# Kernel tuning notes

Measured on AMD Instinct MI355X. Metric: run time of the kernel, lower is better.

## Reference

```python
import jax, jax.numpy as jnp
import numpy as np

B = 2
ROW, COL = 63, 84          # resolution
ROW_, COL_ = 32, 42        # resolution_
N = ROW * COL              # 5292 kv tokens
N_ = ROW_ * COL_           # 1344 q tokens
IN_DIM, OUT_DIM = 256, 512
KEY_DIM, NUM_HEADS, ATTN_RATIO, STRIDE = 16, 8, 2, 2
D = ATTN_RATIO * KEY_DIM   # 32 (value dim per head)
DH = D * NUM_HEADS         # 256
NH_KD = KEY_DIM * NUM_HEADS  # 128
H_KV = DH + NH_KD          # 384
SCALE = KEY_DIM ** -0.5
EPS = 1e-5


def _build_bias_idxs():
    # replicates the itertools.product double loop, vectorized; ids ordered by
    # first occurrence in row-major scan (same as dict insertion order).
    r_ = np.arange(ROW_); c_ = np.arange(COL_)
    r = np.arange(ROW); c = np.arange(COL)
    off_r = np.abs(r_[:, None] * STRIDE - r[None, :])      # (32, 63)
    off_c = np.abs(c_[:, None] * STRIDE - c[None, :])      # (42, 84)
    keys = (off_r[:, None, :, None] * 1000 + off_c[None, :, None, :]).reshape(-1)
    _, first_idx, inv = np.unique(keys, return_index=True, return_inverse=True)
    order = np.argsort(first_idx)
    rank = np.empty_like(order); rank[order] = np.arange(len(order))
    idxs = rank[inv].reshape(N_, N).astype(np.int32)
    return idxs, len(order)


def setup_inputs() -> dict:
    key = jax.random.key(0)
    ks = jax.random.split(key, 12)
    idxs_np, n_off = _build_bias_idxs()
    inp = {
        "x": jax.random.normal(ks[0], (B, N, IN_DIM), jnp.float32),
        "kv_w": jax.random.normal(ks[1], (H_KV, IN_DIM), jnp.float32) * (IN_DIM ** -0.5),
        "kv_g": jnp.ones((H_KV,), jnp.float32),
        "kv_b": jnp.zeros((H_KV,), jnp.float32),
        "q_w": jax.random.normal(ks[2], (NH_KD, IN_DIM), jnp.float32) * (IN_DIM ** -0.5),
        "q_g": jnp.ones((NH_KD,), jnp.float32),
        "q_b": jnp.zeros((NH_KD,), jnp.float32),
        "proj_w": jax.random.normal(ks[3], (OUT_DIM, DH), jnp.float32) * (DH ** -0.5),
        "proj_g": jnp.ones((OUT_DIM,), jnp.float32),
        "proj_b": jnp.zeros((OUT_DIM,), jnp.float32),
        "bias_table": jax.random.normal(ks[4], (NUM_HEADS, n_off), jnp.float32) * 0.02,
        "bias_idxs": jnp.asarray(idxs_np),
    }
    return inp


def _linear_bn(x, w, g, b):
    # Linear (no bias) followed by BatchNorm1d in training mode (batch stats
    # over flattened (B*N) dim, biased variance).
    y = jnp.einsum("bnc,oc->bno", x, w)
    flat = y.reshape(-1, y.shape[-1])
    mu = flat.mean(0)
    var = flat.var(0)
    return (y - mu) * (g / jnp.sqrt(var + EPS)) + b


def _hardswish(x):
    return x * jnp.clip(x + 3.0, 0.0, 6.0) / 6.0


def reference(x, kv_w, kv_g, kv_b, q_w, q_g, q_b, proj_w, proj_g, proj_b,
              bias_table, bias_idxs):
    Bx = x.shape[0]
    # kv projection -> split k (KEY_DIM) and v (D) per head
    kv = _linear_bn(x, kv_w, kv_g, kv_b).reshape(Bx, N, NUM_HEADS, KEY_DIM + D)
    k = kv[..., :KEY_DIM].transpose(0, 2, 1, 3)   # (B, H, N, key_dim)
    v = kv[..., KEY_DIM:].transpose(0, 2, 1, 3)   # (B, H, N, d)
    # q: spatial subsample then projection
    xs = x.reshape(Bx, ROW, COL, IN_DIM)[:, ::STRIDE, ::STRIDE].reshape(Bx, N_, IN_DIM)
    q = _linear_bn(xs, q_w, q_g, q_b).reshape(Bx, N_, NUM_HEADS, KEY_DIM).transpose(0, 2, 1, 3)
    # gathered relative position bias: (H, N_, N)
    ab = bias_table[:, bias_idxs]
    attn = jnp.einsum("bhqd,bhkd->bhqk", q, k) * SCALE + ab[None]
    attn = jax.nn.softmax(attn, axis=-1)
    out = jnp.einsum("bhqk,bhkd->bhqd", attn, v)       # (B, H, N_, d)
    out = out.transpose(0, 2, 1, 3).reshape(Bx, N_, DH)
    out = _linear_bn(_hardswish(out), proj_w, proj_g, proj_b)
    return out
```

## Files before the change

kernel.cpp:

```cpp
#include <hip/hip_runtime.h>
#include <hip/hip_bf16.h>
#include <math.h>

#define N_K 5292
#define N_KP 5376
#define N_Q 1344
#define NH_KD 128
#define NROWS 21504
#define LOG2E 1.4426950408889634f
#define MSTAT 16.0f

typedef float f32x4 __attribute__((ext_vector_type(4)));
typedef short short8 __attribute__((ext_vector_type(8)));

__device__ __forceinline__ float fexp2(float x) {
#if __has_builtin(__builtin_amdgcn_exp2f)
    return __builtin_amdgcn_exp2f(x);
#else
    return exp2f(x);
#endif
}

__device__ __forceinline__ unsigned pk_bf16(float a, float b) {
    union { __hip_bfloat162 h; unsigned u; } c;
    c.h = __float22bfloat162_rn(make_float2(a, b));
    return c.u;
}
__device__ __forceinline__ unsigned short f2bf(float a) {
    return (unsigned short)pk_bf16(a, 0.f);
}

__global__ __launch_bounds__(256) void prep_kernel(
    const float* __restrict__ bias_table, const int* __restrict__ bias_idxs, int n_off,
    float* __restrict__ zbase, unsigned* __restrict__ Vpt32, float* __restrict__ bt_r)
{
    int bid = blockIdx.x;
    const int t = threadIdx.x;
    if (bid < 8) {
        int i = bid * 256 + t;
        if (i < 2048) zbase[i] = 0.f;
        return;
    }
    bid -= 8;
    if (bid < 128) {
        int i = bid * 256 + t;
        int row = i >> 6, c = i & 63;
        Vpt32[(size_t)row * (N_KP / 2) + (5248 / 2) + c] = 0u;
        return;
    }
    bid -= 128;
    {
        int i = bid * 256 + t;
        if (i < 8 * N_K) {
            int h = i / N_K, j = i - h * N_K;
            bt_r[i] = bias_table[h * n_off + bias_idxs[j]] * LOG2E;
        }
    }
}

__device__ __forceinline__ void gemm_body_f32(
    const float* __restrict__ A, const float* __restrict__ W,
    long asrc, int nrow,
    unsigned short (*As)[40], unsigned short (*Bs)[40], f32x4 acc[4])
{
    const int t = threadIdx.x;
    const int w = t >> 6, lane = t & 63, g = lane >> 4, ln = lane & 15;
    const int srow = t >> 2;
    const int sc8 = (t & 3) * 8;

    for (int k0 = 0; k0 < 256; k0 += 32) {
        uint4 a = make_uint4(0, 0, 0, 0);
        if (asrc >= 0) {
            float4 a0 = *(const float4*)(A + asrc * 256 + k0 + sc8);
            float4 a1 = *(const float4*)(A + asrc * 256 + k0 + sc8 + 4);
            a = make_uint4(pk_bf16(a0.x, a0.y), pk_bf16(a0.z, a0.w),
                           pk_bf16(a1.x, a1.y), pk_bf16(a1.z, a1.w));
        }
        float4 b0 = *(const float4*)(W + (size_t)nrow * 256 + k0 + sc8);
        float4 b1 = *(const float4*)(W + (size_t)nrow * 256 + k0 + sc8 + 4);
        uint4 b = make_uint4(pk_bf16(b0.x, b0.y), pk_bf16(b0.z, b0.w),
                             pk_bf16(b1.x, b1.y), pk_bf16(b1.z, b1.w));

        __syncthreads();
        *(uint4*)&As[srow][sc8] = a;
        *(uint4*)&Bs[srow][sc8] = b;
        __syncthreads();

        short8 ah = *(const short8*)&As[w * 16 + ln][g * 8];
        #pragma unroll
        for (int nt = 0; nt < 4; ++nt) {
            short8 bh = *(const short8*)&Bs[nt * 16 + ln][g * 8];
            acc[nt] = __builtin_amdgcn_mfma_f32_16x16x32_bf16(ah, bh, acc[nt], 0, 0, 0);
        }
    }
}

__device__ __forceinline__ void gemm_body_bf16(
    const unsigned short* __restrict__ A, const float* __restrict__ W,
    long asrc, int nrow,
    unsigned short (*As)[40], unsigned short (*Bs)[40], f32x4 acc[4])
{
    const int t = threadIdx.x;
    const int w = t >> 6, lane = t & 63, g = lane >> 4, ln = lane & 15;
    const int srow = t >> 2;
    const int sc8 = (t & 3) * 8;

    for (int k0 = 0; k0 < 256; k0 += 32) {
        uint4 a = *(const uint4*)(A + asrc * 256 + k0 + sc8);
        float4 b0 = *(const float4*)(W + (size_t)nrow * 256 + k0 + sc8);
        float4 b1 = *(const float4*)(W + (size_t)nrow * 256 + k0 + sc8 + 4);
        uint4 b = make_uint4(pk_bf16(b0.x, b0.y), pk_bf16(b0.z, b0.w),
                             pk_bf16(b1.x, b1.y), pk_bf16(b1.z, b1.w));

        __syncthreads();
        *(uint4*)&As[srow][sc8] = a;
        *(uint4*)&Bs[srow][sc8] = b;
        __syncthreads();

        short8 ah = *(const short8*)&As[w * 16 + ln][g * 8];
        #pragma unroll
        for (int nt = 0; nt < 4; ++nt) {
            short8 bh = *(const short8*)&Bs[nt * 16 + ln][g * 8];
            acc[nt] = __builtin_amdgcn_mfma_f32_16x16x32_bf16(ah, bh, acc[nt], 0, 0, 0);
        }
    }
}

__device__ __forceinline__ void gemm_stats(f32x4 acc[4], float* __restrict__ sums,
                                           int n0, int Ncols, float* scratch)
{
    const int t = threadIdx.x;
    const int w = t >> 6, lane = t & 63, g = lane >> 4, ln = lane & 15;
    float s4[4], q4[4];
    #pragma unroll
    for (int nt = 0; nt < 4; ++nt) {
        float s = acc[nt][0] + acc[nt][1] + acc[nt][2] + acc[nt][3];
        float q = fmaf(acc[nt][0], acc[nt][0], fmaf(acc[nt][1], acc[nt][1],
                  fmaf(acc[nt][2], acc[nt][2], acc[nt][3] * acc[nt][3])));
        s += __shfl_xor(s, 16); s += __shfl_xor(s, 32);
        q += __shfl_xor(q, 16); q += __shfl_xor(q, 32);
        s4[nt] = s; q4[nt] = q;
    }
    __syncthreads();
    float* st_s = scratch;
    float* st_q = scratch + 256;
    if (g == 0) {
        #pragma unroll
        for (int nt = 0; nt < 4; ++nt) {
            st_s[(w * 4 + nt) * 16 + ln] = s4[nt];
            st_q[(w * 4 + nt) * 16 + ln] = q4[nt];
        }
    }
    __syncthreads();
    if (t < 64) {
        int nt = t >> 4, c = t & 15;
        float a = 0.f, b2 = 0.f;
        #pragma unroll
        for (int ww = 0; ww < 4; ++ww) {
            a  += st_s[(ww * 4 + nt) * 16 + c];
            b2 += st_q[(ww * 4 + nt) * 16 + c];
        }
        atomicAdd(&sums[n0 + nt * 16 + c], a);
        atomicAdd(&sums[Ncols + n0 + nt * 16 + c], b2);
    }
}

__global__ __launch_bounds__(256) void gemm_qkv(
    const float* __restrict__ X, const float* __restrict__ kv_w, const float* __restrict__ q_w,
    unsigned short* __restrict__ Kp, unsigned short* __restrict__ Vpt,
    float* __restrict__ q_y, float* __restrict__ sums_kv, float* __restrict__ sums_q)
{
    __shared__ unsigned short As[64][40], Bs[64][40];
    const int t = threadIdx.x;
    const int w = t >> 6, lane = t & 63, g = lane >> 4, ln = lane & 15;
    const int srow = t >> 2;
    int id = blockIdx.x;

    f32x4 acc[4];
    #pragma unroll
    for (int nt = 0; nt < 4; ++nt) acc[nt] = (f32x4){0.f, 0.f, 0.f, 0.f};

    if (id < 1008) {
        const int xcd = id & 7, id8 = id >> 3;
        const int my = xcd + (id8 / 6) * 8, ny = id8 % 6;
        if (my >= 166) return;
        const int m0 = my * 64, n0 = ny * 64;
        int mrow = m0 + srow;
        long asrc = (mrow < 10584) ? mrow : -1;
        gemm_body_f32(X, kv_w, asrc, n0 + srow, As, Bs, acc);

        #pragma unroll
        for (int nt = 0; nt < 4; ++nt) {
            int c = n0 + nt * 16 + ln;
            int hh = c / 48, cc = c - 48 * hh;
            #pragma unroll
            for (int reg = 0; reg < 4; ++reg) {
                int mr = m0 + w * 16 + g * 4 + reg;
                if (mr < 10584) {
                    int bb = mr >= N_K;
                    int key = mr - bb * N_K;
                    unsigned short v16 = f2bf(acc[nt][reg]);
                    if (cc < 16) {
                        Kp[((size_t)(bb * 8 + hh) * N_K + key) * 16 + cc] = v16;
                    } else {
                        int kap = key & 63;
                        int keyp = (key & ~63) | (((kap & 15) << 2) | (kap >> 4));
                        Vpt[((size_t)(bb * 8 + hh) * 32 + cc - 16) * N_KP + keyp] = v16;
                    }
                }
            }
        }
        gemm_stats(acc, sums_kv, n0, 384, (float*)&As[0][0]);
    } else {
        id -= 1008;
        const int xcd = id & 7, id8 = id >> 3;
        const int my = xcd + (id8 / 2) * 8, ny = id8 % 2;
        if (my >= 42) return;
        const int m0 = my * 64, n0 = ny * 64;
        int mrow = m0 + srow;
        int bb = mrow / N_Q;
        int i = mrow - bb * N_Q;
        long asrc = (long)(bb * N_K + (i / 42) * 168 + (i % 42) * 2);
        gemm_body_f32(X, q_w, asrc, n0 + srow, As, Bs, acc);

        #pragma unroll
        for (int nt = 0; nt < 4; ++nt)
            #pragma unroll
            for (int reg = 0; reg < 4; ++reg) {
                int mr = m0 + w * 16 + g * 4 + reg;
                q_y[(size_t)mr * 128 + n0 + nt * 16 + ln] = acc[nt][reg];
            }
        gemm_stats(acc, sums_q, n0, 128, (float*)&As[0][0]);
    }
}

__global__ __launch_bounds__(256) void gemm_proj(
    const unsigned short* __restrict__ Ap, const float* __restrict__ Wp,
    float* __restrict__ Y, float* __restrict__ sums)
{
    __shared__ unsigned short As[64][40], Bs[64][40];
    const int t = threadIdx.x;
    const int w = t >> 6, lane = t & 63, g = lane >> 4, ln = lane & 15;
    const int id = blockIdx.x;
    const int xcd = id & 7, id8 = id >> 3;
    const int my = xcd + (id8 / 8) * 8, ny = id8 % 8;
    if (my >= 42) return;
    const int m0 = my * 64, n0 = ny * 64;

    f32x4 acc[4];
    #pragma unroll
    for (int nt = 0; nt < 4; ++nt) acc[nt] = (f32x4){0.f, 0.f, 0.f, 0.f};
    gemm_body_bf16(Ap, Wp, m0 + (t >> 2), n0 + (t >> 2), As, Bs, acc);

    #pragma unroll
    for (int nt = 0; nt < 4; ++nt)
        #pragma unroll
        for (int reg = 0; reg < 4; ++reg) {
            int mr = m0 + w * 16 + g * 4 + reg;
            Y[(size_t)mr * 512 + n0 + nt * 16 + ln] = acc[nt][reg];
        }
    gemm_stats(acc, sums, n0, 512, (float*)&As[0][0]);
}

__global__ __launch_bounds__(256, 5) void attn_mfma(
    const unsigned short* __restrict__ Kp, const unsigned short* __restrict__ Vpt,
    const float* __restrict__ q_y, const float* __restrict__ sums_q,
    const float* __restrict__ q_g, const float* __restrict__ q_b,
    const float* __restrict__ sums_kv, const float* __restrict__ kv_g,
    const float* __restrict__ bt_r,
    float* __restrict__ pl, float* __restrict__ pacc)
{
    const int id = blockIdx.x;
    const int h = id & 7;
    const int z = (id >> 3) & 7;
    const int qt = id >> 6;
    const int b = z >> 2, ks = z & 3;
    const int t = threadIdx.x;
    const int w = t >> 6, lane = t & 63, g = lane >> 4, ln = lane & 15;

    __shared__ unsigned short btm_s[21 * 166];
    __shared__ unsigned short K_s[2][64][24];
    __shared__ unsigned short Vt_s[2][32][72];
    __shared__ unsigned short P_s[4][16][72];

    const int q0 = qt * 64;
    const int kstart = ks * 1344;
    const int kend = (kstart + 1344 < N_K) ? kstart + 1344 : N_K;
    const int ntiles = (kend - kstart + 63) >> 6;
    const bool tail = (ks == 3);

    const int kr0 = kstart / 84;
    const int kr1 = (kend - 1) / 84;
    const int rq2min = (q0 / 42) * 2;
    const int rq2max = ((q0 + 63) / 42) * 2;
    const int dmin_r = rq2min - kr1;
    const int rows = (rq2max - kr0) - dmin_r + 1;
    const int nb = rows * 166;
    const int mx = nb - 1;
    {
        const float* src = bt_r + h * N_K;
        for (int j = t; j < nb; j += 256) {
            int rr = j / 166, ii = j - rr * 166;
            int dr = dmin_r + rr; dr = dr < 0 ? -dr : dr;
            int dc = ii - 83; dc = dc < 0 ? -dc : dc;
            btm_s[j] = f2bf(src[dr * 84 + dc]);
        }
    }

    short8 qfrag = (short8)0;
    if (lane < 32) {
        const float invq = 1.f / 2688.f, invk = 1.f / 10584.f;
        const float post = 0.25f * LOG2E;
        const int c0 = h * 16 + g * 8;
        const int ck = h * 48 + g * 8;
        const float* qp = q_y + (size_t)(b * N_Q + q0 + w * 16 + ln) * NH_KD + c0;
        float vv[8];
        #pragma unroll
        for (int j = 0; j < 8; ++j) {
            float mu  = sums_q[c0 + j] * invq;
            float var = fmaf(-mu, mu, sums_q[128 + c0 + j] * invq);
            float s   = q_g[c0 + j] * rsqrtf(var + 1e-5f) * post;
            float vq  = fmaf(qp[j], s, fmaf(-mu, s, q_b[c0 + j] * post));
            float muk = sums_kv[ck + j] * invk;
            float vrk = fmaf(-muk, muk, sums_kv[384 + ck + j] * invk);
            float sk  = kv_g[ck + j] * rsqrtf(vrk + 1e-5f);
            vv[j] = vq * sk;
        }
        union { short8 s; unsigned u[4]; } qf;
        qf.u[0] = pk_bf16(vv[0], vv[1]); qf.u[1] = pk_bf16(vv[2], vv[3]);
        qf.u[2] = pk_bf16(vv[4], vv[5]); qf.u[3] = pk_bf16(vv[6], vv[7]);
        qfrag = qf.s;
    }

    int base[4];
    #pragma unroll
    for (int reg = 0; reg < 4; ++reg) {
        int qg = q0 + w * 16 + g * 4 + reg;
        int rq2 = (qg / 42) * 2;
        int cq2 = (qg % 42) * 2;
        base[reg] = (rq2 - dmin_r) * 166 + cq2 + 83;
    }
    int off[4], kcc[4];
    #pragma unroll
    for (int st = 0; st < 4; ++st) {
        int kg = kstart + st * 16 + ln;
        int okr = kg / 84;
        kcc[st] = kg - okr * 84;
        off[st] = -(okr * 166 + kcc[st]);
    }

    const unsigned* kp_base = (const unsigned*)Kp + (size_t)(b * 8 + h) * N_K * 8;
    const unsigned short* vp_base = Vpt + (size_t)(b * 8 + h) * 32 * N_KP;
    const int skey = t >> 2, schunk = t & 3;
    const int vrow = t >> 3, vc8 = (t & 7) * 8;

    uint2 kreg; uint4 vreg;
    {
        int kg = kstart + skey; if (kg > N_K - 1) kg = N_K - 1;
        kreg = *(const uint2*)(kp_base + (size_t)kg * 8 + schunk * 2);
        vreg = *(const uint4*)(vp_base + (size_t)vrow * N_KP + kstart + vc8);
    }
    *(uint2*)&K_s[0][skey][schunk * 4] = kreg;
    *(uint4*)&Vt_s[0][vrow][vc8] = vreg;
    __syncthreads();

    float l[4] = {0.f, 0.f, 0.f, 0.f};
    f32x4 acc0 = {0.f, 0.f, 0.f, 0.f}, acc1 = {0.f, 0.f, 0.f, 0.f};
    const f32x4 minit = {-MSTAT, -MSTAT, -MSTAT, -MSTAT};
    int p = 0;

    for (int it = 0; it < ntiles; ++it) {
        const int k0 = kstart + it * 64;
        const bool notlast = (it + 1 < ntiles);
        if (notlast) {
            int kg = k0 + 64 + skey; if (kg > N_K - 1) kg = N_K - 1;
            kreg = *(const uint2*)(kp_base + (size_t)kg * 8 + schunk * 2);
            vreg = *(const uint4*)(vp_base + (size_t)vrow * N_KP + k0 + 64 + vc8);
        }

        f32x4 sf[4];
        #pragma unroll
        for (int st = 0; st < 4; ++st) {
            short8 bf = (short8)0;
            if (lane < 32) bf = *(const short8*)&K_s[p][st * 16 + ln][g * 8];
            sf[st] = __builtin_amdgcn_mfma_f32_16x16x32_bf16(qfrag, bf, minit, 0, 0, 0);
        }

        float pv[4][4];
        #pragma unroll
        for (int st = 0; st < 4; ++st) {
            #pragma unroll
            for (int reg = 0; reg < 4; ++reg) {
                int idx = base[reg] + off[st];
                idx = idx < 0 ? 0 : idx;
                idx = idx > mx ? mx : idx;
                float bias = __uint_as_float(((unsigned)btm_s[idx]) << 16);
                pv[st][reg] = fexp2(sf[st][reg] + bias);
            }
        }
        if (tail && it == ntiles - 1) {
            #pragma unroll
            for (int st = 0; st < 4; ++st) {
                bool bad = (k0 + st * 16 + ln) >= N_K;
                #pragma unroll
                for (int reg = 0; reg < 4; ++reg)
                    pv[st][reg] = bad ? 0.f : pv[st][reg];
            }
        }

        #pragma unroll
        for (int reg = 0; reg < 4; ++reg) {
            l[reg] += (pv[0][reg] + pv[1][reg]) + (pv[2][reg] + pv[3][reg]);
            uint2 pw = make_uint2(pk_bf16(pv[0][reg], pv[1][reg]),
                                  pk_bf16(pv[2][reg], pv[3][reg]));
            *(uint2*)&P_s[w][g * 4 + reg][4 * ln] = pw;
        }
        __asm__ __volatile__("" ::: "memory");

        #pragma unroll
        for (int kt = 0; kt < 2; ++kt) {
            short8 af = *(const short8*)&P_s[w][ln][g * 8 + kt * 32];
            short8 b0 = *(const short8*)&Vt_s[p][ln][g * 8 + kt * 32];
            short8 b1 = *(const short8*)&Vt_s[p][ln + 16][g * 8 + kt * 32];
            acc0 = __builtin_amdgcn_mfma_f32_16x16x32_bf16(af, b0, acc0, 0, 0, 0);
            acc1 = __builtin_amdgcn_mfma_f32_16x16x32_bf16(af, b1, acc1, 0, 0, 0);
        }

        if (notlast) {
            int q2 = p ^ 1;
            *(uint2*)&K_s[q2][skey][schunk * 4] = kreg;
            *(uint4*)&Vt_s[q2][vrow][vc8] = vreg;
            __syncthreads();
            p = q2;
        }

        #pragma unroll
        for (int st = 0; st < 4; ++st) {
            kcc[st] += 64;
            if (kcc[st] >= 84) { kcc[st] -= 84; off[st] -= 146; }
            else off[st] -= 64;
        }
    }

    #pragma unroll
    for (int reg = 0; reg < 4; ++reg) {
        float s = l[reg];
        s += __shfl_xor(s, 1, 16);
        s += __shfl_xor(s, 2, 16);
        s += __shfl_xor(s, 4, 16);
        s += __shfl_xor(s, 8, 16);
        l[reg] = s;
    }

    const int rbase = (b * 8 + h) * N_Q + q0 + w * 16;
    #pragma unroll
    for (int reg = 0; reg < 4; ++reg) {
        int prow = ks * NROWS + rbase + g * 4 + reg;
        pacc[(size_t)prow * 32 + ln]      = acc0[reg];
        pacc[(size_t)prow * 32 + 16 + ln] = acc1[reg];
        if (ln == 0) pl[prow] = l[reg];
    }
}

__global__ __launch_bounds__(256) void combine_kernel(const float* __restrict__ pl,
                                                      const float* __restrict__ pacc,
                                                      const float* __restrict__ sums_kv,
                                                      const float* __restrict__ kv_g,
                                                      const float* __restrict__ kv_b,
                                                      unsigned short* __restrict__ attn_o)
{
    int idx = blockIdx.x * 256 + threadIdx.x;
    int r = idx >> 3, e4 = (idx & 7) * 4;
    float L = (pl[r] + pl[NROWS + r]) + (pl[2 * NROWS + r] + pl[3 * NROWS + r]);
    float invL = 1.f / L;
    size_t o = (size_t)r * 32 + e4;
    float4 v0 = *(const float4*)(pacc + o);
    float4 v1 = *(const float4*)(pacc + (size_t)NROWS * 32 + o);
    float4 v2 = *(const float4*)(pacc + (size_t)2 * NROWS * 32 + o);
    float4 v3 = *(const float4*)(pacc + (size_t)3 * NROWS * 32 + o);
    int q = r % N_Q;
    int bh = r / N_Q;
    int hh = bh & 7, b = bh >> 3;
    const int ch = hh * 48 + 16 + e4;
    const float invk = 1.f / 10584.f;
    float hs[4];
    #pragma unroll
    for (int u = 0; u < 4; ++u) {
        float v = (u == 0 ? v0.x + v1.x + v2.x + v3.x :
                   u == 1 ? v0.y + v1.y + v2.y + v3.y :
                   u == 2 ? v0.z + v1.z + v2.z + v3.z :
                            v0.w + v1.w + v2.w + v3.w);
        float mu  = sums_kv[ch + u] * invk;
        float var = fmaf(-mu, mu, sums_kv[384 + ch + u] * invk);
        float s   = kv_g[ch + u] * rsqrtf(var + 1e-5f);
        float tt  = fmaf(-mu, s, kv_b[ch + u]);
        v = fmaf(s, v * invL, tt);
        hs[u] = v * fminf(fmaxf(v + 3.f, 0.f), 6.f) * (1.f / 6.f);
    }
    *(uint2*)(attn_o + (size_t)(b * N_Q + q) * 256 + hh * 32 + e4) =
        make_uint2(pk_bf16(hs[0], hs[1]), pk_bf16(hs[2], hs[3]));
}

__global__ __launch_bounds__(256) void norm_apply(
    const float* __restrict__ Y, const float* __restrict__ sums,
    const float* __restrict__ g, const float* __restrict__ bb,
    float* __restrict__ out, int rows, int cols, float inv_rows)
{
    __shared__ float sc_s[64], sh_s[64];
    const int t = threadIdx.x;
    const int c0 = blockIdx.x * 64;
    if (t < 64) {
        int c = c0 + t;
        float mu  = sums[c] * inv_rows;
        float var = fmaf(-mu, mu, sums[cols + c] * inv_rows);
        float s   = g[c] * rsqrtf(var + 1e-5f);
        sc_s[t] = s;
        sh_s[t] = fmaf(-mu, s, bb[c]);
    }
    __syncthreads();
    const int c4 = (t & 15) * 4;
    float4 scv = *(const float4*)&sc_s[c4];
    float4 shv = *(const float4*)&sh_s[c4];
    for (int r = blockIdx.y * 16 + (t >> 4); r < rows; r += gridDim.y * 16) {
        size_t off = (size_t)r * cols + c0 + c4;
        float4 v = *(const float4*)(Y + off);
        v.x = fmaf(v.x, scv.x, shv.x);
        v.y = fmaf(v.y, scv.y, shv.y);
        v.z = fmaf(v.z, scv.z, shv.z);
        v.w = fmaf(v.w, scv.w, shv.w);
        *(float4*)(out + off) = v;
    }
}

extern "C" void kernel_launch(void* const* d_in, const int* in_sizes, int n_in,
                              void* d_out, int out_size, void* d_ws, size_t ws_size,
                              hipStream_t stream) {
    (void)n_in; (void)out_size; (void)ws_size;
    const float* x      = (const float*)d_in[0];
    const float* kv_w   = (const float*)d_in[1];
    const float* kv_g   = (const float*)d_in[2];
    const float* kv_b   = (const float*)d_in[3];
    const float* q_w    = (const float*)d_in[4];
    const float* q_g    = (const float*)d_in[5];
    const float* q_b    = (const float*)d_in[6];
    const float* proj_w = (const float*)d_in[7];
    const float* proj_g = (const float*)d_in[8];
    const float* proj_b = (const float*)d_in[9];
    const float* bias_table = (const float*)d_in[10];
    const int*   bias_idxs  = (const int*)d_in[11];
    const int    n_off = in_sizes[10] / 8;
    float* out = (float*)d_out;

    float* ws = (float*)d_ws;
    float* q_y  = ws;
    float* pacc = q_y + 2688 * 128;
    float* proj_y = pacc;
    float* pl = pacc + 4 * NROWS * 32;
    unsigned short* attn_o = (unsigned short*)(pl + 4 * NROWS);
    unsigned short* Kp  = attn_o + 2688 * 256;
    unsigned short* Vpt = Kp + 2 * 8 * N_K * 16;
    float* zbase   = (float*)(Vpt + 2 * 8 * 32 * N_KP);
    float* sums_kv = zbase;
    float* sums_q  = sums_kv + 768;
    float* sums_p  = sums_q + 256;
    float* bt_r    = sums_p + 1024;

    prep_kernel<<<302, 256, 0, stream>>>(bias_table, bias_idxs, n_off, zbase,
                                         (unsigned*)Vpt, bt_r);
    gemm_qkv<<<1104, 256, 0, stream>>>(x, kv_w, q_w, Kp, Vpt, q_y, sums_kv, sums_q);
    attn_mfma<<<1344, 256, 0, stream>>>(Kp, Vpt, q_y, sums_q, q_g, q_b,
                                        sums_kv, kv_g, bt_r, pl, pacc);
    combine_kernel<<<672, 256, 0, stream>>>(pl, pacc, sums_kv, kv_g, kv_b, attn_o);
    gemm_proj<<<384, 256, 0, stream>>>(attn_o, proj_w, proj_y, sums_p);
    norm_apply<<<dim3(8, 84), 256, 0, stream>>>(proj_y, sums_p, proj_g, proj_b, out,
                                                2688, 512, 1.f / 2688.f);
}
```

Baseline: 198.8 us.

## Fuse split-K combine into attention; load K/V fragments directly from global

Restructures the attention kernel so each block takes 16 queries, with its four waves splitting the key range. Partial sums are reduced in shared memory and the BN/hardswish epilogue is applied in the same kernel, which removes the separate combine kernel and the global pacc/pl round trip. K/V fragments are loaded straight from global memory into registers with ping-pong double buffering, replacing the LDS staging and its per-tile barriers. The prep kernel is folded into extra blocks of the QKV GEMM that prebuild a bf16 bias matrix in global memory, and the stats buffer is cleared with a memset. The trade-offs are more global K/V traffic per block, a larger bias LDS footprint, and occupancy lowered from 5 to 4.

```diff
diff --git a/kernel.cpp b/kernel.cpp
--- a/kernel.cpp
+++ b/kernel.cpp
@@ -6,9 +6,9 @@
 #define N_KP 5376
 #define N_Q 1344
 #define NH_KD 128
-#define NROWS 21504
 #define LOG2E 1.4426950408889634f
 #define MSTAT 16.0f
+#define BTM_H 20750
 
 typedef float f32x4 __attribute__((ext_vector_type(4)));
 typedef short short8 __attribute__((ext_vector_type(8)));
@@ -28,34 +28,6 @@
 }
 __device__ __forceinline__ unsigned short f2bf(float a) {
     return (unsigned short)pk_bf16(a, 0.f);
-}
-
-__global__ __launch_bounds__(256) void prep_kernel(
-    const float* __restrict__ bias_table, const int* __restrict__ bias_idxs, int n_off,
-    float* __restrict__ zbase, unsigned* __restrict__ Vpt32, float* __restrict__ bt_r)
-{
-    int bid = blockIdx.x;
-    const int t = threadIdx.x;
-    if (bid < 8) {
-        int i = bid * 256 + t;
-        if (i < 2048) zbase[i] = 0.f;
-        return;
-    }
-    bid -= 8;
-    if (bid < 128) {
-        int i = bid * 256 + t;
-        int row = i >> 6, c = i & 63;
-        Vpt32[(size_t)row * (N_KP / 2) + (5248 / 2) + c] = 0u;
-        return;
-    }
-    bid -= 128;
-    {
-        int i = bid * 256 + t;
-        if (i < 8 * N_K) {
-            int h = i / N_K, j = i - h * N_K;
-            bt_r[i] = bias_table[h * n_off + bias_idxs[j]] * LOG2E;
-        }
-    }
 }
 
 __device__ __forceinline__ void gemm_body_f32(
@@ -167,7 +139,9 @@
 
 __global__ __launch_bounds__(256) void gemm_qkv(
     const float* __restrict__ X, const float* __restrict__ kv_w, const float* __restrict__ q_w,
+    const float* __restrict__ bias_table, const int* __restrict__ bias_idxs, int n_off,
     unsigned short* __restrict__ Kp, unsigned short* __restrict__ Vpt,
+    unsigned short* __restrict__ btm_g,
     float* __restrict__ q_y, float* __restrict__ sums_kv, float* __restrict__ sums_q)
 {
     __shared__ unsigned short As[64][40], Bs[64][40];
@@ -175,6 +149,32 @@
     const int w = t >> 6, lane = t & 63, g = lane >> 4, ln = lane & 15;
     const int srow = t >> 2;
     int id = blockIdx.x;
+
+    if (id >= 1104) {
+        id -= 1104;
+        if (id < 168) {
+            int i = id * 256 + t;
+            int row = i / 84, j = i - row * 84;
+            int slot;
+            if (j < 20) {
+                int kap = 44 + j;
+                slot = 5248 + (((kap & 15) << 2) | (kap >> 4));
+            } else {
+                slot = 5312 + (j - 20);
+            }
+            Vpt[(size_t)row * N_KP + slot] = 0;
+        } else {
+            int i = (id - 168) * 256 + t;
+            if (i < 8 * BTM_H) {
+                int h = i / BTM_H, r = i - h * BTM_H;
+                int dri = r / 166, dci = r - dri * 166;
+                int dr = dri - 62; dr = dr < 0 ? -dr : dr;
+                int dc = dci - 83; dc = dc < 0 ? -dc : dc;
+                btm_g[i] = f2bf(bias_table[h * n_off + bias_idxs[dr * 84 + dc]] * LOG2E);
+            }
+        }
+        return;
+    }
 
     f32x4 acc[4];
     #pragma unroll
@@ -262,49 +262,116 @@
     gemm_stats(acc, sums, n0, 512, (float*)&As[0][0]);
 }
 
-__global__ __launch_bounds__(256, 5) void attn_mfma(
+
+struct Frags { short8 kf[4]; short8 v0[2]; short8 v1[2]; };
+
+__device__ __forceinline__ void load_frags(
+    Frags& f, int k0, int lane, int g, int ln,
+    const unsigned short* __restrict__ kp_base,
+    const unsigned short* __restrict__ vrow0,
+    const unsigned short* __restrict__ vrow1)
+{
+    #pragma unroll
+    for (int st = 0; st < 4; ++st) {
+        int kg = k0 + st * 16 + ln;
+        kg = kg > N_K - 1 ? N_K - 1 : kg;
+        f.kf[st] = (lane < 32) ? *(const short8*)(kp_base + (size_t)kg * 16 + g * 8)
+                               : (short8)0;
+    }
+    #pragma unroll
+    for (int kt = 0; kt < 2; ++kt) {
+        f.v0[kt] = *(const short8*)(vrow0 + k0 + kt * 32 + g * 8);
+        f.v1[kt] = *(const short8*)(vrow1 + k0 + kt * 32 + g * 8);
+    }
+}
+
+__device__ __forceinline__ void do_tile(
+    const Frags& f, int k0, bool mask, int kend_mask,
+    const short8& qfrag, const int base[4], int off[4], int kcc[4],
+    const unsigned short* __restrict__ btm_s, int mx,
+    int w, int g, int ln, unsigned short (*P_s)[16][72],
+    float l[4], f32x4& acc0, f32x4& acc1)
+{
+    const f32x4 minit = {-MSTAT, -MSTAT, -MSTAT, -MSTAT};
+    f32x4 sf[4];
+    #pragma unroll
+    for (int st = 0; st < 4; ++st)
+        sf[st] = __builtin_amdgcn_mfma_f32_16x16x32_bf16(qfrag, f.kf[st], minit, 0, 0, 0);
+
+    float pv[4][4];
+    #pragma unroll
+    for (int st = 0; st < 4; ++st) {
+        #pragma unroll
+        for (int reg = 0; reg < 4; ++reg) {
+            int idx = base[reg] + off[st];
+            idx = idx < 0 ? 0 : idx;
+            idx = idx > mx ? mx : idx;
+            float bias = __uint_as_float(((unsigned)btm_s[idx]) << 16);
+            pv[st][reg] = fexp2(sf[st][reg] + bias);
+        }
+    }
+    if (mask) {
+        #pragma unroll
+        for (int st = 0; st < 4; ++st) {
+            bool bad = (k0 + st * 16 + ln) >= kend_mask;
+            #pragma unroll
+            for (int reg = 0; reg < 4; ++reg)
+                pv[st][reg] = bad ? 0.f : pv[st][reg];
+        }
+    }
+
+    #pragma unroll
+    for (int reg = 0; reg < 4; ++reg) {
+        l[reg] += (pv[0][reg] + pv[1][reg]) + (pv[2][reg] + pv[3][reg]);
+        uint2 pw = make_uint2(pk_bf16(pv[0][reg], pv[1][reg]),
+                              pk_bf16(pv[2][reg], pv[3][reg]));
+        *(uint2*)&P_s[w][g * 4 + reg][4 * ln] = pw;
+    }
+    __asm__ __volatile__("" ::: "memory");
+
+    #pragma unroll
+    for (int kt = 0; kt < 2; ++kt) {
+        short8 af = *(const short8*)&P_s[w][ln][g * 8 + kt * 32];
+        acc0 = __builtin_amdgcn_mfma_f32_16x16x32_bf16(af, f.v0[kt], acc0, 0, 0, 0);
+        acc1 = __builtin_amdgcn_mfma_f32_16x16x32_bf16(af, f.v1[kt], acc1, 0, 0, 0);
+    }
+
+    #pragma unroll
+    for (int st = 0; st < 4; ++st) {
+        kcc[st] += 64;
+        if (kcc[st] >= 84) { kcc[st] -= 84; off[st] -= 146; }
+        else off[st] -= 64;
+    }
+}
+
+__global__ __launch_bounds__(256, 4) void attn_mfma(
     const unsigned short* __restrict__ Kp, const unsigned short* __restrict__ Vpt,
     const float* __restrict__ q_y, const float* __restrict__ sums_q,
     const float* __restrict__ q_g, const float* __restrict__ q_b,
     const float* __restrict__ sums_kv, const float* __restrict__ kv_g,
-    const float* __restrict__ bt_r,
-    float* __restrict__ pl, float* __restrict__ pacc)
+    const float* __restrict__ kv_b, const unsigned short* __restrict__ btm_g,
+    unsigned short* __restrict__ attn_o)
 {
     const int id = blockIdx.x;
     const int h = id & 7;
-    const int z = (id >> 3) & 7;
-    const int qt = id >> 6;
-    const int b = z >> 2, ks = z & 3;
+    const int b = (id >> 3) & 1;
+    const int qt = id >> 4;
     const int t = threadIdx.x;
     const int w = t >> 6, lane = t & 63, g = lane >> 4, ln = lane & 15;
 
-    __shared__ unsigned short btm_s[21 * 166];
-    __shared__ unsigned short K_s[2][64][24];
-    __shared__ unsigned short Vt_s[2][32][72];
+    __shared__ unsigned short btm_s[65 * 166];
     __shared__ unsigned short P_s[4][16][72];
 
-    const int q0 = qt * 64;
-    const int kstart = ks * 1344;
-    const int kend = (kstart + 1344 < N_K) ? kstart + 1344 : N_K;
-    const int ntiles = (kend - kstart + 63) >> 6;
-    const bool tail = (ks == 3);
-
-    const int kr0 = kstart / 84;
-    const int kr1 = (kend - 1) / 84;
+    const int q0 = qt * 16;
     const int rq2min = (q0 / 42) * 2;
-    const int rq2max = ((q0 + 63) / 42) * 2;
-    const int dmin_r = rq2min - kr1;
-    const int rows = (rq2max - kr0) - dmin_r + 1;
-    const int nb = rows * 166;
-    const int mx = nb - 1;
+    const int rq2max = ((q0 + 15) / 42) * 2;
+    const int rows = rq2max - rq2min + 63;
+    const int nb2 = rows * 83;
+    const int mx = rows * 166 - 1;
     {
-        const float* src = bt_r + h * N_K;
-        for (int j = t; j < nb; j += 256) {
-            int rr = j / 166, ii = j - rr * 166;
-            int dr = dmin_r + rr; dr = dr < 0 ? -dr : dr;
-            int dc = ii - 83; dc = dc < 0 ? -dc : dc;
-            btm_s[j] = f2bf(src[dr * 84 + dc]);
-        }
+        const unsigned* src = (const unsigned*)(btm_g + h * BTM_H + rq2min * 166);
+        unsigned* dst = (unsigned*)btm_s;
+        for (int j = t; j < nb2; j += 256) dst[j] = src[j];
     }
 
     short8 qfrag = (short8)0;
@@ -313,7 +380,7 @@
         const float post = 0.25f * LOG2E;
         const int c0 = h * 16 + g * 8;
         const int ck = h * 48 + g * 8;
-        const float* qp = q_y + (size_t)(b * N_Q + q0 + w * 16 + ln) * NH_KD + c0;
+        const float* qp = q_y + (size_t)(b * N_Q + q0 + ln) * NH_KD + c0;
         float vv[8];
         #pragma unroll
         for (int j = 0; j < 8; ++j) {
@@ -332,14 +399,20 @@
         qfrag = qf.s;
     }
 
+    const int dmin_r = rq2min - 62;
     int base[4];
     #pragma unroll
     for (int reg = 0; reg < 4; ++reg) {
-        int qg = q0 + w * 16 + g * 4 + reg;
+        int qg = q0 + g * 4 + reg;
         int rq2 = (qg / 42) * 2;
         int cq2 = (qg % 42) * 2;
         base[reg] = (rq2 - dmin_r) * 166 + cq2 + 83;
     }
+
+    const int kstart = w * 1344;
+    const int ntiles = (w < 3) ? 21 : 20;
+    const bool tailw = (w == 3);
+
     int off[4], kcc[4];
     #pragma unroll
     for (int st = 0; st < 4; ++st) {
@@ -349,97 +422,30 @@
         off[st] = -(okr * 166 + kcc[st]);
     }
 
-    const unsigned* kp_base = (const unsigned*)Kp + (size_t)(b * 8 + h) * N_K * 8;
-    const unsigned short* vp_base = Vpt + (size_t)(b * 8 + h) * 32 * N_KP;
-    const int skey = t >> 2, schunk = t & 3;
-    const int vrow = t >> 3, vc8 = (t & 7) * 8;
-
-    uint2 kreg; uint4 vreg;
-    {
-        int kg = kstart + skey; if (kg > N_K - 1) kg = N_K - 1;
-        kreg = *(const uint2*)(kp_base + (size_t)kg * 8 + schunk * 2);
-        vreg = *(const uint4*)(vp_base + (size_t)vrow * N_KP + kstart + vc8);
-    }
-    *(uint2*)&K_s[0][skey][schunk * 4] = kreg;
-    *(uint4*)&Vt_s[0][vrow][vc8] = vreg;
+    const unsigned short* kp_base = Kp + (size_t)(b * 8 + h) * N_K * 16;
+    const unsigned short* vp = Vpt + (size_t)(b * 8 + h) * 32 * N_KP;
+    const unsigned short* vrow0 = vp + (size_t)ln * N_KP;
+    const unsigned short* vrow1 = vp + (size_t)(ln + 16) * N_KP;
+
     __syncthreads();
 
     float l[4] = {0.f, 0.f, 0.f, 0.f};
     f32x4 acc0 = {0.f, 0.f, 0.f, 0.f}, acc1 = {0.f, 0.f, 0.f, 0.f};
-    const f32x4 minit = {-MSTAT, -MSTAT, -MSTAT, -MSTAT};
-    int p = 0;
-
-    for (int it = 0; it < ntiles; ++it) {
-        const int k0 = kstart + it * 64;
-        const bool notlast = (it + 1 < ntiles);
-        if (notlast) {
-            int kg = k0 + 64 + skey; if (kg > N_K - 1) kg = N_K - 1;
-            kreg = *(const uint2*)(kp_base + (size_t)kg * 8 + schunk * 2);
-            vreg = *(const uint4*)(vp_base + (size_t)vrow * N_KP + k0 + 64 + vc8);
-        }
-
-        f32x4 sf[4];
-        #pragma unroll
-        for (int st = 0; st < 4; ++st) {
-            short8 bf = (short8)0;
-            if (lane < 32) bf = *(const short8*)&K_s[p][st * 16 + ln][g * 8];
-            sf[st] = __builtin_amdgcn_mfma_f32_16x16x32_bf16(qfrag, bf, minit, 0, 0, 0);
-        }
-
-        float pv[4][4];
-        #pragma unroll
-        for (int st = 0; st < 4; ++st) {
-            #pragma unroll
-            for (int reg = 0; reg < 4; ++reg) {
-                int idx = base[reg] + off[st];
-                idx = idx < 0 ? 0 : idx;
-                idx = idx > mx ? mx : idx;
-                float bias = __uint_as_float(((unsigned)btm_s[idx]) << 16);
-                pv[st][reg] = fexp2(sf[st][reg] + bias);
-            }
-        }
-        if (tail && it == ntiles - 1) {
-            #pragma unroll
-            for (int st = 0; st < 4; ++st) {
-                bool bad = (k0 + st * 16 + ln) >= N_K;
-                #pragma unroll
-                for (int reg = 0; reg < 4; ++reg)
-                    pv[st][reg] = bad ? 0.f : pv[st][reg];
-            }
-        }
-
-        #pragma unroll
-        for (int reg = 0; reg < 4; ++reg) {
-            l[reg] += (pv[0][reg] + pv[1][reg]) + (pv[2][reg] + pv[3][reg]);
-            uint2 pw = make_uint2(pk_bf16(pv[0][reg], pv[1][reg]),
-                                  pk_bf16(pv[2][reg], pv[3][reg]));
-            *(uint2*)&P_s[w][g * 4 + reg][4 * ln] = pw;
-        }
-        __asm__ __volatile__("" ::: "memory");
-
-        #pragma unroll
-        for (int kt = 0; kt < 2; ++kt) {
-            short8 af = *(const short8*)&P_s[w][ln][g * 8 + kt * 32];
-            short8 b0 = *(const short8*)&Vt_s[p][ln][g * 8 + kt * 32];
-            short8 b1 = *(const short8*)&Vt_s[p][ln + 16][g * 8 + kt * 32];
-            acc0 = __builtin_amdgcn_mfma_f32_16x16x32_bf16(af, b0, acc0, 0, 0, 0);
-            acc1 = __builtin_amdgcn_mfma_f32_16x16x32_bf16(af, b1, acc1, 0, 0, 0);
-        }
-
-        if (notlast) {
-            int q2 = p ^ 1;
-            *(uint2*)&K_s[q2][skey][schunk * 4] = kreg;
-            *(uint4*)&Vt_s[q2][vrow][vc8] = vreg;
-            __syncthreads();
-            p = q2;
-        }
-
-        #pragma unroll
-        for (int st = 0; st < 4; ++st) {
-            kcc[st] += 64;
-            if (kcc[st] >= 84) { kcc[st] -= 84; off[st] -= 146; }
-            else off[st] -= 64;
-        }
+
+    Frags fA, fB;
+    load_frags(fA, kstart, lane, g, ln, kp_base, vrow0, vrow1);
+    int it = 0;
+    while (true) {
+        int k0 = kstart + it * 64;
+        if (it + 1 < ntiles) load_frags(fB, k0 + 64, lane, g, ln, kp_base, vrow0, vrow1);
+        do_tile(fA, k0, tailw && (it == ntiles - 1), N_K, qfrag, base, off, kcc,
+                btm_s, mx, w, g, ln, P_s, l, acc0, acc1);
+        if (++it >= ntiles) break;
+        k0 += 64;
+        if (it + 1 < ntiles) load_frags(fA, k0 + 64, lane, g, ln, kp_base, vrow0, vrow1);
+        do_tile(fB, k0, tailw && (it == ntiles - 1), N_K, qfrag, base, off, kcc,
+                btm_s, mx, w, g, ln, P_s, l, acc0, acc1);
+        if (++it >= ntiles) break;
     }
 
     #pragma unroll
@@ -452,53 +458,45 @@
         l[reg] = s;
     }
 
-    const int rbase = (b * 8 + h) * N_Q + q0 + w * 16;
+    __syncthreads();
+    float* accs = (float*)btm_s;
+    float* ls   = accs + 4 * 16 * 32;
     #pragma unroll
     for (int reg = 0; reg < 4; ++reg) {
-        int prow = ks * NROWS + rbase + g * 4 + reg;
-        pacc[(size_t)prow * 32 + ln]      = acc0[reg];
-        pacc[(size_t)prow * 32 + 16 + ln] = acc1[reg];
-        if (ln == 0) pl[prow] = l[reg];
-    }
-}
-
-__global__ __launch_bounds__(256) void combine_kernel(const float* __restrict__ pl,
-                                                      const float* __restrict__ pacc,
-                                                      const float* __restrict__ sums_kv,
-                                                      const float* __restrict__ kv_g,
-                                                      const float* __restrict__ kv_b,
-                                                      unsigned short* __restrict__ attn_o)
-{
-    int idx = blockIdx.x * 256 + threadIdx.x;
-    int r = idx >> 3, e4 = (idx & 7) * 4;
-    float L = (pl[r] + pl[NROWS + r]) + (pl[2 * NROWS + r] + pl[3 * NROWS + r]);
-    float invL = 1.f / L;
-    size_t o = (size_t)r * 32 + e4;
-    float4 v0 = *(const float4*)(pacc + o);
-    float4 v1 = *(const float4*)(pacc + (size_t)NROWS * 32 + o);
-    float4 v2 = *(const float4*)(pacc + (size_t)2 * NROWS * 32 + o);
-    float4 v3 = *(const float4*)(pacc + (size_t)3 * NROWS * 32 + o);
-    int q = r % N_Q;
-    int bh = r / N_Q;
-    int hh = bh & 7, b = bh >> 3;
-    const int ch = hh * 48 + 16 + e4;
-    const float invk = 1.f / 10584.f;
-    float hs[4];
-    #pragma unroll
-    for (int u = 0; u < 4; ++u) {
-        float v = (u == 0 ? v0.x + v1.x + v2.x + v3.x :
-                   u == 1 ? v0.y + v1.y + v2.y + v3.y :
-                   u == 2 ? v0.z + v1.z + v2.z + v3.z :
-                            v0.w + v1.w + v2.w + v3.w);
-        float mu  = sums_kv[ch + u] * invk;
-        float var = fmaf(-mu, mu, sums_kv[384 + ch + u] * invk);
-        float s   = kv_g[ch + u] * rsqrtf(var + 1e-5f);
-        float tt  = fmaf(-mu, s, kv_b[ch + u]);
-        v = fmaf(s, v * invL, tt);
-        hs[u] = v * fminf(fmaxf(v + 3.f, 0.f), 6.f) * (1.f / 6.f);
-    }
-    *(uint2*)(attn_o + (size_t)(b * N_Q + q) * 256 + hh * 32 + e4) =
-        make_uint2(pk_bf16(hs[0], hs[1]), pk_bf16(hs[2], hs[3]));
+        int qrow = g * 4 + reg;
+        accs[((w * 16 + qrow) * 32) + ln]      = acc0[reg];
+        accs[((w * 16 + qrow) * 32) + 16 + ln] = acc1[reg];
+        if (ln == 0) ls[w * 16 + qrow] = l[reg];
+    }
+    __syncthreads();
+
+    if (t < 128) {
+        int q = t >> 3, e4 = (t & 7) * 4;
+        float L = (ls[q] + ls[16 + q]) + (ls[32 + q] + ls[48 + q]);
+        float invL = 1.f / L;
+        float4 s0 = *(const float4*)&accs[(q)* 32 + e4];
+        float4 s1 = *(const float4*)&accs[(16 + q) * 32 + e4];
+        float4 s2 = *(const float4*)&accs[(32 + q) * 32 + e4];
+        float4 s3 = *(const float4*)&accs[(48 + q) * 32 + e4];
+        const int ch = h * 48 + 16 + e4;
+        const float invk = 1.f / 10584.f;
+        float hs[4];
+        #pragma unroll
+        for (int u = 0; u < 4; ++u) {
+            float v = (u == 0 ? s0.x + s1.x + s2.x + s3.x :
+                       u == 1 ? s0.y + s1.y + s2.y + s3.y :
+                       u == 2 ? s0.z + s1.z + s2.z + s3.z :
+                                s0.w + s1.w + s2.w + s3.w);
+            float mu  = sums_kv[ch + u] * invk;
+            float var = fmaf(-mu, mu, sums_kv[384 + ch + u] * invk);
+            float sc  = kv_g[ch + u] * rsqrtf(var + 1e-5f);
+            float tt  = fmaf(-mu, sc, kv_b[ch + u]);
+            v = fmaf(sc, v * invL, tt);
+            hs[u] = v * fminf(fmaxf(v + 3.f, 0.f), 6.f) * (1.f / 6.f);
+        }
+        *(uint2*)(attn_o + (size_t)(b * N_Q + q0 + q) * 256 + h * 32 + e4) =
+            make_uint2(pk_bf16(hs[0], hs[1]), pk_bf16(hs[2], hs[3]));
+    }
 }
 
 __global__ __launch_bounds__(256) void norm_apply(
@@ -552,25 +550,22 @@
     float* out = (float*)d_out;
 
     float* ws = (float*)d_ws;
-    float* q_y  = ws;
-    float* pacc = q_y + 2688 * 128;
-    float* proj_y = pacc;
-    float* pl = pacc + 4 * NROWS * 32;
-    unsigned short* attn_o = (unsigned short*)(pl + 4 * NROWS);
+    float* q_y    = ws;
+    float* proj_y = q_y + 2688 * 128;
+    unsigned short* attn_o = (unsigned short*)(proj_y + 2688 * 512);
     unsigned short* Kp  = attn_o + 2688 * 256;
     unsigned short* Vpt = Kp + 2 * 8 * N_K * 16;
-    float* zbase   = (float*)(Vpt + 2 * 8 * 32 * N_KP);
-    float* sums_kv = zbase;
+    unsigned short* btm_g = Vpt + 2 * 8 * 32 * N_KP;
+    float* sums_kv = (float*)(btm_g + 8 * BTM_H);
     float* sums_q  = sums_kv + 768;
     float* sums_p  = sums_q + 256;
-    float* bt_r    = sums_p + 1024;
-
-    prep_kernel<<<302, 256, 0, stream>>>(bias_table, bias_idxs, n_off, zbase,
-                                         (unsigned*)Vpt, bt_r);
-    gemm_qkv<<<1104, 256, 0, stream>>>(x, kv_w, q_w, Kp, Vpt, q_y, sums_kv, sums_q);
+
+    hipMemsetAsync(sums_kv, 0, 2048 * sizeof(float), stream);
+    gemm_qkv<<<1104 + 168 + 649, 256, 0, stream>>>(x, kv_w, q_w, bias_table, bias_idxs,
+                                                   n_off, Kp, Vpt, btm_g,
+                                                   q_y, sums_kv, sums_q);
     attn_mfma<<<1344, 256, 0, stream>>>(Kp, Vpt, q_y, sums_q, q_g, q_b,
-                                        sums_kv, kv_g, bt_r, pl, pacc);
-    combine_kernel<<<672, 256, 0, stream>>>(pl, pacc, sums_kv, kv_g, kv_b, attn_o);
+                                        sums_kv, kv_g, kv_b, btm_g, attn_o);
     gemm_proj<<<384, 256, 0, stream>>>(attn_o, proj_w, proj_y, sums_p);
     norm_apply<<<dim3(8, 84), 256, 0, stream>>>(proj_y, sums_p, proj_g, proj_b, out,
                                                 2688, 512, 1.f / 2688.f);
```

Measured after the change: 226.7 us. +14.0%, slower.
